# Optimization experiments

Hardware: AMD Instinct MI355X
Metric: run time of the kernel (lower is better)

## Reference

```python
import jax, jax.numpy as jnp
import numpy as np

NO_EDGE_OFFSET_T_NORM = 1.0    # added to the no_edge branch for the T-norm (min) operator
NO_EDGE_OFFSET_T_CONORM = -1.0  # added to the no_edge branch for the T-conorm (max) operator

B, IN_F, OUT_F = 2048, 256, 256
N_EDGE_TYPES, N_OPS = 2, 2


def setup_inputs() -> dict:
    key = jax.random.key(0)
    k1, k2, k3 = jax.random.split(key, 3)
    x = jax.random.uniform(k1, (B, IN_F), dtype=jnp.float32)
    prob_edge_weights = jax.random.normal(k2, (OUT_F, IN_F, N_EDGE_TYPES), dtype=jnp.float32)
    prob_node_weights = jax.random.normal(k3, (OUT_F, N_OPS), dtype=jnp.float32)
    return {"x": x, "prob_edge_weights": prob_edge_weights, "prob_node_weights": prob_node_weights}


def reference(x, prob_edge_weights, prob_node_weights):
    # train_mode = train_both: softmax over edge types and over operators
    edge_prob = jax.nn.softmax(prob_edge_weights, axis=-1)  # [O, I, E]
    node_prob = jax.nn.softmax(prob_node_weights, axis=-1)  # [O, U]

    p_edge = edge_prob[:, :, 0]     # prob of real edge (identity transform), [O, I]
    p_noedge = edge_prob[:, :, 1]   # prob of no_edge (zeros + operator-specific offset), [O, I]

    # expected edge value per (batch, out, in); the no_edge branch contributes
    # offset * p_noedge since its edge_value is zeros(x) + offset.
    base = x[:, None, :] * p_edge   # [B, O, I]

    # operator 0: T-norm (min over in_features), no_edge offset = +1
    ev_min = jnp.min(base + NO_EDGE_OFFSET_T_NORM * p_noedge, axis=-1)    # [B, O]
    # operator 1: T-conorm (max over in_features), no_edge offset = -1
    ev_max = jnp.max(base + NO_EDGE_OFFSET_T_CONORM * p_noedge, axis=-1)  # [B, O]

    # expectation over operators
    return ev_min * node_prob[:, 0] + ev_max * node_prob[:, 1]  # [B, O]
```

## Files before the change

kernel.cpp:

```cpp
#include <hip/hip_runtime.h>
#include <math.h>

#define IN_F  256
#define OUT_F 256
#define OTILE 64
#define BTILE 8
#define NTH   256

typedef _Float16 h2 __attribute__((ext_vector_type(2)));

__global__ __launch_bounds__(NTH, 4)
void den_kernel(const float* __restrict__ x,
                const float* __restrict__ pew,
                const float* __restrict__ pnw,
                float* __restrict__ out)
{
    __shared__ __align__(16) _Float16 pe_lds[OTILE * IN_F];

    const int tid = threadIdx.x;
    const int b0  = blockIdx.x * BTILE;
    const int o0  = blockIdx.y * OTILE;

    {
        const int r16 = tid >> 4;
        const int c   = tid & 15;
        for (int rg = 0; rg < 4; ++rg) {
            const int o  = rg * 16 + r16;
            const int sw = (o & 15) << 3;
            const float4* wp = reinterpret_cast<const float4*>(pew + (size_t)(o0 + o) * (IN_F * 2));
            char* rowp = reinterpret_cast<char*>(&pe_lds[o * IN_F]);
            #pragma unroll
            for (int k = 0; k < 8; ++k) {
                float4 w = wp[k * 16 + c];
                float pe0 = __builtin_amdgcn_rcpf(1.0f + __expf(w.y - w.x));
                float pe1 = __builtin_amdgcn_rcpf(1.0f + __expf(w.w - w.z));
                const int byteoff = (4 * (k * 16 + c)) ^ sw;
                h2 pv; pv.x = (_Float16)pe0; pv.y = (_Float16)pe1;
                *reinterpret_cast<h2*>(rowp + byteoff) = pv;
            }
        }
    }
    __syncthreads();

    const int lane = tid & 63;
    const int wid  = tid >> 6;
    const int bb0  = b0 + wid * 2;
    const char* rowp = reinterpret_cast<const char*>(&pe_lds[lane * IN_F]);
    const int sw = (lane & 15) << 3;

    const h2 two2 = {(_Float16)2.0f, (_Float16)2.0f};
    h2 mn[2], mx[2];
    #pragma unroll
    for (int j = 0; j < 2; ++j) {
        mn[j].x = mn[j].y = (_Float16)INFINITY;
        mx[j].x = mx[j].y = (_Float16)(-INFINITY);
    }

    const float* xr0 = x + (size_t)bb0 * IN_F;

    #pragma unroll 4
    for (int c = 0; c < 64; ++c) {
        h2 pA = *reinterpret_cast<const h2*>(rowp + ((8 * c) ^ sw));
        h2 pB = *reinterpret_cast<const h2*>(rowp + (((8 * c) ^ sw) + 4));
        #pragma unroll
        for (int j = 0; j < 2; ++j) {
            float4 xv = *reinterpret_cast<const float4*>(xr0 + j * IN_F + 4 * c);
            h2 xA; xA.x = (_Float16)xv.x; xA.y = (_Float16)xv.y;
            h2 xB; xB.x = (_Float16)xv.z; xB.y = (_Float16)xv.w;
            h2 tA = __builtin_elementwise_fma(xA, pA, -pA);
            h2 tB = __builtin_elementwise_fma(xB, pB, -pB);
            h2 uA = __builtin_elementwise_fma(two2, pA, tA);
            h2 uB = __builtin_elementwise_fma(two2, pB, tB);
            mn[j] = __builtin_elementwise_min(mn[j], __builtin_elementwise_min(tA, tB));
            mx[j] = __builtin_elementwise_max(mx[j], __builtin_elementwise_max(uA, uB));
        }
    }

    const int o = o0 + lane;
    float2 nw = *reinterpret_cast<const float2*>(pnw + 2 * (size_t)o);
    float n0 = __builtin_amdgcn_rcpf(1.0f + __expf(nw.y - nw.x));
    float n1 = 1.0f - n0;
    #pragma unroll
    for (int j = 0; j < 2; ++j) {
        float mnf = fminf((float)mn[j].x, (float)mn[j].y);
        float mxf = fmaxf((float)mx[j].x, (float)mx[j].y);
        out[(size_t)(bb0 + j) * OUT_F + o] = (mnf + 1.0f) * n0 + (mxf - 1.0f) * n1;
    }
}

extern "C" void kernel_launch(void* const* d_in, const int* in_sizes, int n_in,
                              void* d_out, int out_size, void* d_ws, size_t ws_size,
                              hipStream_t stream) {
    (void)d_ws; (void)ws_size; (void)n_in; (void)out_size;
    const float* x   = (const float*)d_in[0];
    const float* pew = (const float*)d_in[1];
    const float* pnw = (const float*)d_in[2];
    float* out = (float*)d_out;
    const int B = in_sizes[0] / IN_F;
    dim3 grid(B / BTILE, OUT_F / OTILE);
    den_kernel<<<grid, NTH, 0, stream>>>(x, pew, pnw, out);
}
```

Measured before the change: 77.48 us.

## Precompute fp16 edge probabilities and fp16 x in a prep kernel

Adds a prep kernel that computes the edge softmax once into fp16 and converts x to fp16 in workspace. The main kernel then copies precomputed half-precision probabilities into LDS instead of redoing exp/rcp per block, and reads half-width x rows with no per-iteration conversion. This removes redundant transcendental work (each weight tile was recomputed by every batch block) and halves x traffic. The cost is an extra launch and a round trip through workspace memory.

```diff
diff --git a/kernel.cpp b/kernel.cpp
--- a/kernel.cpp
+++ b/kernel.cpp
@@ -8,14 +8,40 @@
 #define NTH   256
 
 typedef _Float16 h2 __attribute__((ext_vector_type(2)));
+union u32h2 { unsigned int u; h2 h; };
+
+__global__ __launch_bounds__(256)
+void prep_kernel(const float* __restrict__ x,
+                 const float* __restrict__ pew,
+                 unsigned int* __restrict__ pe16,
+                 uint2* __restrict__ x16)
+{
+    const int bid = blockIdx.x;
+    const int t   = threadIdx.x;
+    if (bid < 128) {
+        const int idx = bid * 256 + t;
+        float4 w = reinterpret_cast<const float4*>(pew)[idx];
+        float pe0 = __builtin_amdgcn_rcpf(1.0f + __expf(w.y - w.x));
+        float pe1 = __builtin_amdgcn_rcpf(1.0f + __expf(w.w - w.z));
+        u32h2 r; r.h.x = (_Float16)pe0; r.h.y = (_Float16)pe1;
+        pe16[idx] = r.u;
+    } else {
+        const int idx = (bid - 128) * 256 + t;
+        float4 v = reinterpret_cast<const float4*>(x)[idx];
+        u32h2 a, b;
+        a.h.x = (_Float16)v.x; a.h.y = (_Float16)v.y;
+        b.h.x = (_Float16)v.z; b.h.y = (_Float16)v.w;
+        x16[idx] = make_uint2(a.u, b.u);
+    }
+}
 
 __global__ __launch_bounds__(NTH, 4)
-void den_kernel(const float* __restrict__ x,
-                const float* __restrict__ pew,
-                const float* __restrict__ pnw,
-                float* __restrict__ out)
+void den_main(const unsigned int* __restrict__ pe16,
+              const uint2* __restrict__ x16,
+              const float* __restrict__ pnw,
+              float* __restrict__ out)
 {
-    __shared__ __align__(16) _Float16 pe_lds[OTILE * IN_F];
+    __shared__ __align__(16) unsigned int pe_lds[OTILE * (IN_F / 2)];
 
     const int tid = threadIdx.x;
     const int b0  = blockIdx.x * BTILE;
@@ -24,28 +50,25 @@
     {
         const int r16 = tid >> 4;
         const int c   = tid & 15;
+        #pragma unroll
         for (int rg = 0; rg < 4; ++rg) {
             const int o  = rg * 16 + r16;
             const int sw = (o & 15) << 3;
-            const float4* wp = reinterpret_cast<const float4*>(pew + (size_t)(o0 + o) * (IN_F * 2));
-            char* rowp = reinterpret_cast<char*>(&pe_lds[o * IN_F]);
+            const uint2* src = reinterpret_cast<const uint2*>(pe16 + (size_t)(o0 + o) * (IN_F / 2));
+            char* rowp = reinterpret_cast<char*>(&pe_lds[o * (IN_F / 2)]);
             #pragma unroll
-            for (int k = 0; k < 8; ++k) {
-                float4 w = wp[k * 16 + c];
-                float pe0 = __builtin_amdgcn_rcpf(1.0f + __expf(w.y - w.x));
-                float pe1 = __builtin_amdgcn_rcpf(1.0f + __expf(w.w - w.z));
-                const int byteoff = (4 * (k * 16 + c)) ^ sw;
-                h2 pv; pv.x = (_Float16)pe0; pv.y = (_Float16)pe1;
-                *reinterpret_cast<h2*>(rowp + byteoff) = pv;
+            for (int q = 0; q < 4; ++q) {
+                uint2 v = src[c * 4 + q];
+                *reinterpret_cast<uint2*>(rowp + ((c * 32 + q * 8) ^ sw)) = v;
             }
         }
     }
     __syncthreads();
 
     const int lane = tid & 63;
-    const int wid  = tid >> 6;
+    const int wid  = __builtin_amdgcn_readfirstlane(tid >> 6);
     const int bb0  = b0 + wid * 2;
-    const char* rowp = reinterpret_cast<const char*>(&pe_lds[lane * IN_F]);
+    const char* rowp = reinterpret_cast<const char*>(&pe_lds[lane * (IN_F / 2)]);
     const int sw = (lane & 15) << 3;
 
     const h2 two2 = {(_Float16)2.0f, (_Float16)2.0f};
@@ -56,23 +79,35 @@
         mx[j].x = mx[j].y = (_Float16)(-INFINITY);
     }
 
-    const float* xr0 = x + (size_t)bb0 * IN_F;
+    const uint2* xr0 = x16 + (size_t)bb0 * (IN_F / 4);
+    const uint2* xr1 = x16 + (size_t)(bb0 + 1) * (IN_F / 4);
 
     #pragma unroll 4
     for (int c = 0; c < 64; ++c) {
-        h2 pA = *reinterpret_cast<const h2*>(rowp + ((8 * c) ^ sw));
-        h2 pB = *reinterpret_cast<const h2*>(rowp + (((8 * c) ^ sw) + 4));
-        #pragma unroll
-        for (int j = 0; j < 2; ++j) {
-            float4 xv = *reinterpret_cast<const float4*>(xr0 + j * IN_F + 4 * c);
-            h2 xA; xA.x = (_Float16)xv.x; xA.y = (_Float16)xv.y;
-            h2 xB; xB.x = (_Float16)xv.z; xB.y = (_Float16)xv.w;
-            h2 tA = __builtin_elementwise_fma(xA, pA, -pA);
-            h2 tB = __builtin_elementwise_fma(xB, pB, -pB);
+        uint2 pv = *reinterpret_cast<const uint2*>(rowp + ((8 * c) ^ sw));
+        u32h2 pa, pb; pa.u = pv.x; pb.u = pv.y;
+        const h2 pA = pa.h, pB = pb.h;
+
+        uint2 xc0 = xr0[c];
+        uint2 xc1 = xr1[c];
+        u32h2 t0a, t0b, t1a, t1b;
+        t0a.u = xc0.x; t0b.u = xc0.y; t1a.u = xc1.x; t1b.u = xc1.y;
+
+        {
+            h2 tA = __builtin_elementwise_fma(t0a.h, pA, -pA);
+            h2 tB = __builtin_elementwise_fma(t0b.h, pB, -pB);
             h2 uA = __builtin_elementwise_fma(two2, pA, tA);
             h2 uB = __builtin_elementwise_fma(two2, pB, tB);
-            mn[j] = __builtin_elementwise_min(mn[j], __builtin_elementwise_min(tA, tB));
-            mx[j] = __builtin_elementwise_max(mx[j], __builtin_elementwise_max(uA, uB));
+            mn[0] = __builtin_elementwise_min(mn[0], __builtin_elementwise_min(tA, tB));
+            mx[0] = __builtin_elementwise_max(mx[0], __builtin_elementwise_max(uA, uB));
+        }
+        {
+            h2 tA = __builtin_elementwise_fma(t1a.h, pA, -pA);
+            h2 tB = __builtin_elementwise_fma(t1b.h, pB, -pB);
+            h2 uA = __builtin_elementwise_fma(two2, pA, tA);
+            h2 uB = __builtin_elementwise_fma(two2, pB, tB);
+            mn[1] = __builtin_elementwise_min(mn[1], __builtin_elementwise_min(tA, tB));
+            mx[1] = __builtin_elementwise_max(mx[1], __builtin_elementwise_max(uA, uB));
         }
     }
 
@@ -84,19 +119,25 @@
     for (int j = 0; j < 2; ++j) {
         float mnf = fminf((float)mn[j].x, (float)mn[j].y);
         float mxf = fmaxf((float)mx[j].x, (float)mx[j].y);
-        out[(size_t)(bb0 + j) * OUT_F + o] = (mnf + 1.0f) * n0 + (mxf - 1.0f) * n1;
+        out[(size_t)(b0 + wid * 2 + j) * OUT_F + o] = (mnf + 1.0f) * n0 + (mxf - 1.0f) * n1;
     }
 }
 
 extern "C" void kernel_launch(void* const* d_in, const int* in_sizes, int n_in,
                               void* d_out, int out_size, void* d_ws, size_t ws_size,
                               hipStream_t stream) {
-    (void)d_ws; (void)ws_size; (void)n_in; (void)out_size;
+    (void)ws_size; (void)n_in; (void)out_size;
     const float* x   = (const float*)d_in[0];
     const float* pew = (const float*)d_in[1];
     const float* pnw = (const float*)d_in[2];
     float* out = (float*)d_out;
+
+    unsigned int* pe16 = (unsigned int*)d_ws;
+    uint2*        x16  = (uint2*)((char*)d_ws + 131072);
+
+    prep_kernel<<<640, 256, 0, stream>>>(x, pew, pe16, x16);
+
     const int B = in_sizes[0] / IN_F;
     dim3 grid(B / BTILE, OUT_F / OTILE);
-    den_kernel<<<grid, NTH, 0, stream>>>(x, pew, pnw, out);
+    den_main<<<grid, NTH, 0, stream>>>(pe16, x16, pnw, out);
 }
```

Result: faster. 71.16 us (-8.2%).

## Replace XOR-swizzled LDS layout with padded rows and widen LDS/x loads

Applied to the files above, without the earlier changes.

Changes the shared-memory layout of edge probabilities from an XOR swizzle to padded rows (stride 264 halves), so each lane can read 16 bytes per LDS access instead of two 4-byte reads. The prologue now has each thread convert 8 consecutive float4 weights and write them contiguously. The main loop processes 8 inputs per iteration, converts x with packed round-toward-zero conversion, and makes the wave id uniform via readfirstlane. The aim is fewer LDS and conversion instructions, at the cost of a slightly larger LDS footprint, possible bank conflicts in the new write pattern, and different rounding of x to fp16.

```diff
diff --git a/kernel.cpp b/kernel.cpp
--- a/kernel.cpp
+++ b/kernel.cpp
@@ -6,6 +6,7 @@
 #define OTILE 64
 #define BTILE 8
 #define NTH   256
+#define PSTRIDE 264
 
 typedef _Float16 h2 __attribute__((ext_vector_type(2)));
 
@@ -15,7 +16,7 @@
                 const float* __restrict__ pnw,
                 float* __restrict__ out)
 {
-    __shared__ __align__(16) _Float16 pe_lds[OTILE * IN_F];
+    __shared__ __align__(16) _Float16 pe_lds[OTILE * PSTRIDE];
 
     const int tid = threadIdx.x;
     const int b0  = blockIdx.x * BTILE;
@@ -24,29 +25,31 @@
     {
         const int r16 = tid >> 4;
         const int c   = tid & 15;
+        #pragma unroll
         for (int rg = 0; rg < 4; ++rg) {
-            const int o  = rg * 16 + r16;
-            const int sw = (o & 15) << 3;
-            const float4* wp = reinterpret_cast<const float4*>(pew + (size_t)(o0 + o) * (IN_F * 2));
-            char* rowp = reinterpret_cast<char*>(&pe_lds[o * IN_F]);
+            const int o = rg * 16 + r16;
+            const float4* wp = reinterpret_cast<const float4*>(pew + (size_t)(o0 + o) * (IN_F * 2)) + c * 8;
+            h2 v[8];
             #pragma unroll
             for (int k = 0; k < 8; ++k) {
-                float4 w = wp[k * 16 + c];
+                float4 w = wp[k];
                 float pe0 = __builtin_amdgcn_rcpf(1.0f + __expf(w.y - w.x));
                 float pe1 = __builtin_amdgcn_rcpf(1.0f + __expf(w.w - w.z));
-                const int byteoff = (4 * (k * 16 + c)) ^ sw;
-                h2 pv; pv.x = (_Float16)pe0; pv.y = (_Float16)pe1;
-                *reinterpret_cast<h2*>(rowp + byteoff) = pv;
+                v[k].x = (_Float16)pe0; v[k].y = (_Float16)pe1;
             }
+            _Float16* dst = &pe_lds[o * PSTRIDE + c * 16];
+            reinterpret_cast<h2*>(dst)[0] = v[0];  reinterpret_cast<h2*>(dst)[1] = v[1];
+            reinterpret_cast<h2*>(dst)[2] = v[2];  reinterpret_cast<h2*>(dst)[3] = v[3];
+            reinterpret_cast<h2*>(dst)[4] = v[4];  reinterpret_cast<h2*>(dst)[5] = v[5];
+            reinterpret_cast<h2*>(dst)[6] = v[6];  reinterpret_cast<h2*>(dst)[7] = v[7];
         }
     }
     __syncthreads();
 
     const int lane = tid & 63;
-    const int wid  = tid >> 6;
+    const int wid  = __builtin_amdgcn_readfirstlane(tid >> 6);
     const int bb0  = b0 + wid * 2;
-    const char* rowp = reinterpret_cast<const char*>(&pe_lds[lane * IN_F]);
-    const int sw = (lane & 15) << 3;
+    const _Float16* rowp = &pe_lds[lane * PSTRIDE];
 
     const h2 two2 = {(_Float16)2.0f, (_Float16)2.0f};
     h2 mn[2], mx[2];
@@ -56,23 +59,38 @@
         mx[j].x = mx[j].y = (_Float16)(-INFINITY);
     }
 
-    const float* xr0 = x + (size_t)bb0 * IN_F;
+    const float4* xr0 = reinterpret_cast<const float4*>(x + (size_t)(bb0 + 0) * IN_F);
+    const float4* xr1 = reinterpret_cast<const float4*>(x + (size_t)(bb0 + 1) * IN_F);
 
-    #pragma unroll 4
-    for (int c = 0; c < 64; ++c) {
-        h2 pA = *reinterpret_cast<const h2*>(rowp + ((8 * c) ^ sw));
-        h2 pB = *reinterpret_cast<const h2*>(rowp + (((8 * c) ^ sw) + 4));
+    #pragma unroll 8
+    for (int c = 0; c < 32; ++c) {
+        h2 p[4];
+        *reinterpret_cast<float4*>(p) = *reinterpret_cast<const float4*>(rowp + c * 8);
+
         #pragma unroll
         for (int j = 0; j < 2; ++j) {
-            float4 xv = *reinterpret_cast<const float4*>(xr0 + j * IN_F + 4 * c);
-            h2 xA; xA.x = (_Float16)xv.x; xA.y = (_Float16)xv.y;
-            h2 xB; xB.x = (_Float16)xv.z; xB.y = (_Float16)xv.w;
-            h2 tA = __builtin_elementwise_fma(xA, pA, -pA);
-            h2 tB = __builtin_elementwise_fma(xB, pB, -pB);
-            h2 uA = __builtin_elementwise_fma(two2, pA, tA);
-            h2 uB = __builtin_elementwise_fma(two2, pB, tB);
-            mn[j] = __builtin_elementwise_min(mn[j], __builtin_elementwise_min(tA, tB));
-            mx[j] = __builtin_elementwise_max(mx[j], __builtin_elementwise_max(uA, uB));
+            const float4* xr = j ? xr1 : xr0;
+            float4 xa = xr[c * 2 + 0];
+            float4 xb = xr[c * 2 + 1];
+            h2 xh[4];
+            xh[0] = __builtin_bit_cast(h2, __builtin_amdgcn_cvt_pkrtz(xa.x, xa.y));
+            xh[1] = __builtin_bit_cast(h2, __builtin_amdgcn_cvt_pkrtz(xa.z, xa.w));
+            xh[2] = __builtin_bit_cast(h2, __builtin_amdgcn_cvt_pkrtz(xb.x, xb.y));
+            xh[3] = __builtin_bit_cast(h2, __builtin_amdgcn_cvt_pkrtz(xb.z, xb.w));
+            h2 t0 = __builtin_elementwise_fma(xh[0], p[0], -p[0]);
+            h2 t1 = __builtin_elementwise_fma(xh[1], p[1], -p[1]);
+            h2 t2 = __builtin_elementwise_fma(xh[2], p[2], -p[2]);
+            h2 t3 = __builtin_elementwise_fma(xh[3], p[3], -p[3]);
+            h2 u0 = __builtin_elementwise_fma(two2, p[0], t0);
+            h2 u1 = __builtin_elementwise_fma(two2, p[1], t1);
+            h2 u2 = __builtin_elementwise_fma(two2, p[2], t2);
+            h2 u3 = __builtin_elementwise_fma(two2, p[3], t3);
+            mn[j] = __builtin_elementwise_min(mn[j],
+                      __builtin_elementwise_min(__builtin_elementwise_min(t0, t1),
+                                                __builtin_elementwise_min(t2, t3)));
+            mx[j] = __builtin_elementwise_max(mx[j],
+                      __builtin_elementwise_max(__builtin_elementwise_max(u0, u1),
+                                                __builtin_elementwise_max(u2, u3)));
         }
     }
 
```

New measurement: 79.26 us. 2.3% more time.

## Precompute fp16 edge probabilities and x in a prep kernel, drop LDS staging

Applied to the files above, without the earlier changes.

Adds a prep kernel that computes the softmax edge probabilities once and converts x to packed fp16, writing both to workspace in a transposed, coalesced layout. Before this, every block recomputed the probabilities for its 64 output rows into LDS. The main kernel now drops the shared-memory stage and the barrier, reading 16-byte packed fp16 vectors straight from global/L2 for both weights and x. The cost is an extra kernel launch and a round trip through workspace memory.

```diff
diff --git a/kernel.cpp b/kernel.cpp
--- a/kernel.cpp
+++ b/kernel.cpp
@@ -8,45 +8,58 @@
 #define NTH   256
 
 typedef _Float16 h2 __attribute__((ext_vector_type(2)));
+union u4h { uint4 u; h2 h[4]; };
+
+__global__ __launch_bounds__(256)
+void prep_kernel(const float* __restrict__ x,
+                 const float* __restrict__ pew,
+                 uint4* __restrict__ pe16,
+                 uint4* __restrict__ x16)
+{
+    const int bid = blockIdx.x;
+    const int t   = threadIdx.x;
+    if (bid < 32) {
+        const int c = bid;
+        const int o = t;
+        const float4* wp = reinterpret_cast<const float4*>(pew) + (size_t)o * 128 + c * 4;
+        u4h r;
+        #pragma unroll
+        for (int q = 0; q < 4; ++q) {
+            float4 w = wp[q];
+            float pe0 = __builtin_amdgcn_rcpf(1.0f + __expf(w.y - w.x));
+            float pe1 = __builtin_amdgcn_rcpf(1.0f + __expf(w.w - w.z));
+            r.h[q].x = (_Float16)pe0; r.h[q].y = (_Float16)pe1;
+        }
+        pe16[c * 256 + o] = r.u;
+    } else {
+        const int u = (bid - 32) * 256 + t;
+        const float4* xp = reinterpret_cast<const float4*>(x) + (size_t)u * 2;
+        float4 a = xp[0], b = xp[1];
+        u4h r;
+        r.h[0] = __builtin_bit_cast(h2, __builtin_amdgcn_cvt_pkrtz(a.x, a.y));
+        r.h[1] = __builtin_bit_cast(h2, __builtin_amdgcn_cvt_pkrtz(a.z, a.w));
+        r.h[2] = __builtin_bit_cast(h2, __builtin_amdgcn_cvt_pkrtz(b.x, b.y));
+        r.h[3] = __builtin_bit_cast(h2, __builtin_amdgcn_cvt_pkrtz(b.z, b.w));
+        x16[u] = r.u;
+    }
+}
 
 __global__ __launch_bounds__(NTH, 4)
-void den_kernel(const float* __restrict__ x,
-                const float* __restrict__ pew,
-                const float* __restrict__ pnw,
-                float* __restrict__ out)
+void den_main(const uint4* __restrict__ pe16,
+              const uint4* __restrict__ x16,
+              const float* __restrict__ pnw,
+              float* __restrict__ out)
 {
-    __shared__ __align__(16) _Float16 pe_lds[OTILE * IN_F];
+    const int tid  = threadIdx.x;
+    const int lane = tid & 63;
+    const int wid  = __builtin_amdgcn_readfirstlane(tid >> 6);
+    const int b0   = blockIdx.x * BTILE;
+    const int o0   = blockIdx.y * OTILE;
+    const int bb0  = b0 + wid * 2;
 
-    const int tid = threadIdx.x;
-    const int b0  = blockIdx.x * BTILE;
-    const int o0  = blockIdx.y * OTILE;
-
-    {
-        const int r16 = tid >> 4;
-        const int c   = tid & 15;
-        for (int rg = 0; rg < 4; ++rg) {
-            const int o  = rg * 16 + r16;
-            const int sw = (o & 15) << 3;
-            const float4* wp = reinterpret_cast<const float4*>(pew + (size_t)(o0 + o) * (IN_F * 2));
-            char* rowp = reinterpret_cast<char*>(&pe_lds[o * IN_F]);
-            #pragma unroll
-            for (int k = 0; k < 8; ++k) {
-                float4 w = wp[k * 16 + c];
-                float pe0 = __builtin_amdgcn_rcpf(1.0f + __expf(w.y - w.x));
-                float pe1 = __builtin_amdgcn_rcpf(1.0f + __expf(w.w - w.z));
-                const int byteoff = (4 * (k * 16 + c)) ^ sw;
-                h2 pv; pv.x = (_Float16)pe0; pv.y = (_Float16)pe1;
-                *reinterpret_cast<h2*>(rowp + byteoff) = pv;
-            }
-        }
-    }
-    __syncthreads();
-
-    const int lane = tid & 63;
-    const int wid  = tid >> 6;
-    const int bb0  = b0 + wid * 2;
-    const char* rowp = reinterpret_cast<const char*>(&pe_lds[lane * IN_F]);
-    const int sw = (lane & 15) << 3;
+    const uint4* per = pe16 + o0 + lane;
+    const uint4* xr0 = x16 + (size_t)(bb0 + 0) * 32;
+    const uint4* xr1 = x16 + (size_t)(bb0 + 1) * 32;
 
     const h2 two2 = {(_Float16)2.0f, (_Float16)2.0f};
     h2 mn[2], mx[2];
@@ -56,23 +69,43 @@
         mx[j].x = mx[j].y = (_Float16)(-INFINITY);
     }
 
-    const float* xr0 = x + (size_t)bb0 * IN_F;
+    #pragma unroll 4
+    for (int c = 0; c < 32; ++c) {
+        u4h p;  p.u  = per[c * 256];
+        u4h xa; xa.u = xr0[c];
+        u4h xb; xb.u = xr1[c];
 
-    #pragma unroll 4
-    for (int c = 0; c < 64; ++c) {
-        h2 pA = *reinterpret_cast<const h2*>(rowp + ((8 * c) ^ sw));
-        h2 pB = *reinterpret_cast<const h2*>(rowp + (((8 * c) ^ sw) + 4));
-        #pragma unroll
-        for (int j = 0; j < 2; ++j) {
-            float4 xv = *reinterpret_cast<const float4*>(xr0 + j * IN_F + 4 * c);
-            h2 xA; xA.x = (_Float16)xv.x; xA.y = (_Float16)xv.y;
-            h2 xB; xB.x = (_Float16)xv.z; xB.y = (_Float16)xv.w;
-            h2 tA = __builtin_elementwise_fma(xA, pA, -pA);
-            h2 tB = __builtin_elementwise_fma(xB, pB, -pB);
-            h2 uA = __builtin_elementwise_fma(two2, pA, tA);
-            h2 uB = __builtin_elementwise_fma(two2, pB, tB);
-            mn[j] = __builtin_elementwise_min(mn[j], __builtin_elementwise_min(tA, tB));
-            mx[j] = __builtin_elementwise_max(mx[j], __builtin_elementwise_max(uA, uB));
+        {
+            h2 t0 = __builtin_elementwise_fma(xa.h[0], p.h[0], -p.h[0]);
+            h2 t1 = __builtin_elementwise_fma(xa.h[1], p.h[1], -p.h[1]);
+            h2 t2 = __builtin_elementwise_fma(xa.h[2], p.h[2], -p.h[2]);
+            h2 t3 = __builtin_elementwise_fma(xa.h[3], p.h[3], -p.h[3]);
+            h2 u0 = __builtin_elementwise_fma(two2, p.h[0], t0);
+            h2 u1 = __builtin_elementwise_fma(two2, p.h[1], t1);
+            h2 u2 = __builtin_elementwise_fma(two2, p.h[2], t2);
+            h2 u3 = __builtin_elementwise_fma(two2, p.h[3], t3);
+            mn[0] = __builtin_elementwise_min(mn[0],
+                      __builtin_elementwise_min(__builtin_elementwise_min(t0, t1),
+                                                __builtin_elementwise_min(t2, t3)));
+            mx[0] = __builtin_elementwise_max(mx[0],
+                      __builtin_elementwise_max(__builtin_elementwise_max(u0, u1),
+                                                __builtin_elementwise_max(u2, u3)));
+        }
+        {
+            h2 t0 = __builtin_elementwise_fma(xb.h[0], p.h[0], -p.h[0]);
+            h2 t1 = __builtin_elementwise_fma(xb.h[1], p.h[1], -p.h[1]);
+            h2 t2 = __builtin_elementwise_fma(xb.h[2], p.h[2], -p.h[2]);
+            h2 t3 = __builtin_elementwise_fma(xb.h[3], p.h[3], -p.h[3]);
+            h2 u0 = __builtin_elementwise_fma(two2, p.h[0], t0);
+            h2 u1 = __builtin_elementwise_fma(two2, p.h[1], t1);
+            h2 u2 = __builtin_elementwise_fma(two2, p.h[2], t2);
+            h2 u3 = __builtin_elementwise_fma(two2, p.h[3], t3);
+            mn[1] = __builtin_elementwise_min(mn[1],
+                      __builtin_elementwise_min(__builtin_elementwise_min(t0, t1),
+                                                __builtin_elementwise_min(t2, t3)));
+            mx[1] = __builtin_elementwise_max(mx[1],
+                      __builtin_elementwise_max(__builtin_elementwise_max(u0, u1),
+                                                __builtin_elementwise_max(u2, u3)));
         }
     }
 
@@ -91,12 +124,18 @@
 extern "C" void kernel_launch(void* const* d_in, const int* in_sizes, int n_in,
                               void* d_out, int out_size, void* d_ws, size_t ws_size,
                               hipStream_t stream) {
-    (void)d_ws; (void)ws_size; (void)n_in; (void)out_size;
+    (void)ws_size; (void)n_in; (void)out_size;
     const float* x   = (const float*)d_in[0];
     const float* pew = (const float*)d_in[1];
     const float* pnw = (const float*)d_in[2];
     float* out = (float*)d_out;
+
+    uint4* pe16 = (uint4*)d_ws;
+    uint4* x16  = (uint4*)((char*)d_ws + 131072);
+
+    prep_kernel<<<288, 256, 0, stream>>>(x, pew, pe16, x16);
+
     const int B = in_sizes[0] / IN_F;
     dim3 grid(B / BTILE, OUT_F / OTILE);
-    den_kernel<<<grid, NTH, 0, stream>>>(x, pew, pnw, out);
+    den_main<<<grid, NTH, 0, stream>>>(pe16, x16, pnw, out);
 }
```

Result: faster. 70.50 us (-9.0%).
